# Performance work log

Measured on AMD Instinct MI355X. Metric: run time of the kernel, lower is better.

The kernel has to match this reference:

```python
import jax, jax.numpy as jnp
import numpy as np
from jax import lax

LN_EPS = 1e-5

def _conv1d(h, w, b):
    # h: [N, L, Cin], w: [Cout, Cin, K] (torch Conv1d layout), padding=1
    out = lax.conv_general_dilated(h, w, window_strides=(1,), padding=[(1, 1)],
                                   dimension_numbers=("NWC", "OIW", "NWC"))
    return out + b

def _layer_norm(h, g, b):
    m = jnp.mean(h, axis=-1, keepdims=True)
    v = jnp.mean((h - m) ** 2, axis=-1, keepdims=True)
    return (h - m) * lax.rsqrt(v + LN_EPS) * g + b

def setup_inputs() -> dict:
    key = jax.random.key(0)
    ks = jax.random.split(key, 8)
    N, L, D, F = 32, 512, 384, 256
    return {
        "x": jax.random.normal(ks[0], (N, L, D), jnp.float32),
        "conv1_w": jax.random.normal(ks[1], (F, D, 3), jnp.float32) * 0.05,
        "conv1_b": jnp.zeros((F,), jnp.float32),
        "ln1_g": jnp.ones((F,), jnp.float32),
        "ln1_b": jnp.zeros((F,), jnp.float32),
        "conv2_w": jax.random.normal(ks[2], (F, F, 3), jnp.float32) * 0.05,
        "conv2_b": jnp.zeros((F,), jnp.float32),
        "ln2_g": jnp.ones((F,), jnp.float32),
        "ln2_b": jnp.zeros((F,), jnp.float32),
        "lin_w": jax.random.normal(ks[3], (F,), jnp.float32) * 0.05,
        "lin_b": jnp.zeros((), jnp.float32),
        "target": jax.random.randint(ks[4], (N, L), 0, 8, dtype=jnp.int32),
        "mel_max_length": 2048,
    }

def reference(x, conv1_w, conv1_b, ln1_g, ln1_b, conv2_w, conv2_b, ln2_g, ln2_b,
              lin_w, lin_b, target, mel_max_length):
    # Duration predictor (dropout is identity at inference)
    h = jax.nn.relu(_layer_norm(_conv1d(x, conv1_w, conv1_b), ln1_g, ln1_b))
    h = jax.nn.relu(_layer_norm(_conv1d(h, conv2_w, conv2_b), ln2_g, ln2_b))
    duration_predictor_output = jnp.einsum("nlf,f->nl", h, lin_w) + lin_b  # [N, L]

    # LR: frame t copies phoneme j iff cumsum(dur)[:j] <= t < cumsum(dur)[:j+1]
    # (equivalent to the one-hot alignment matmul, padded to mel_max_length)
    N, L, D = x.shape
    T = mel_max_length
    cums = jnp.cumsum(target, axis=-1)                      # [N, L]
    frames = jnp.arange(T, dtype=cums.dtype)                # [T]
    idx = jax.vmap(lambda c: jnp.searchsorted(c, frames, side="right"))(cums)  # [N, T]
    valid = frames[None, :] < cums[:, -1:]                  # frames beyond total are zero
    gathered = jnp.take_along_axis(x, jnp.clip(idx, 0, L - 1)[:, :, None], axis=1)
    output = gathered * valid[:, :, None].astype(x.dtype)   # [N, T, D]
    return output, duration_predictor_output
```

## Files before the change

kernel.cpp:

```cpp
#include <hip/hip_runtime.h>
#include <hip/hip_bf16.h>

#define NB   32
#define TMEL 2048

typedef unsigned short u16;
typedef short s8v __attribute__((ext_vector_type(8)));
typedef float f4v __attribute__((ext_vector_type(4)));
typedef u16 u16x8 __attribute__((ext_vector_type(8)));

static __device__ __forceinline__ u16 f2bf(float v) {
    __hip_bfloat16 h = __float2bfloat16(v);
    return *(u16*)&h;
}

__global__ __launch_bounds__(256) void gather_prep_kernel(
    const float* __restrict__ x,
    const int*   __restrict__ target,
    const float* __restrict__ w1,
    const float* __restrict__ w2,
    u16* __restrict__ Wt1,
    u16* __restrict__ Wt2,
    u16* __restrict__ zbuf,
    float* __restrict__ out0)
{
    __shared__ int c[512];
    __shared__ int ridx[64];
    const int b = blockIdx.x, tid = threadIdx.x;

    if (b >= 1024) {
        if (b == 1024 && tid < 8) {
            u16x8 z = {0, 0, 0, 0, 0, 0, 0, 0};
            *(u16x8*)(zbuf + tid * 8) = z;
        }
        if (b < 2176) {
            const int K = 1152, DIN = 384;
            int e = (b - 1024) * 256 + tid;
            int f = e / K;
            int rem = e - f * K;
            int kc = rem / DIN;
            int d = rem - kc * DIN;
            Wt1[e] = f2bf(w1[f * K + d * 3 + kc]);
        } else {
            const int K = 768, DIN = 256;
            int e = (b - 2176) * 256 + tid;
            int f = e / K;
            int rem = e - f * K;
            int kc = rem / DIN;
            int d = rem - kc * DIN;
            Wt2[e] = f2bf(w2[f * K + d * 3 + kc]);
        }
        return;
    }

    const int n = b >> 5, sub = b & 31;
    c[tid]       = target[n * 512 + tid];
    c[tid + 256] = target[n * 512 + 256 + tid];
    __syncthreads();
    for (int off = 1; off < 512; off <<= 1) {
        int v0 = (tid       >= off) ? c[tid       - off] : 0;
        int v1 = (tid + 256 >= off) ? c[tid + 256 - off] : 0;
        __syncthreads();
        c[tid]       += v0;
        c[tid + 256] += v1;
        __syncthreads();
    }
    const int total = c[511];
    if (tid < 64) {
        int t = sub * 64 + tid;
        int lo = 0, hi = 512;
        while (lo < hi) {
            int mid = (lo + hi) >> 1;
            if (c[mid] <= t) lo = mid + 1; else hi = mid;
        }
        ridx[tid] = (t < total) ? min(lo, 511) : -1;
    }
    __syncthreads();

    const size_t xbase = (size_t)(n << 9) * 384;
    const size_t obase = ((size_t)(n << 11) + sub * 64) * 384;
    #pragma unroll 4
    for (int it = 0; it < 12; ++it) {
        int u  = tid + it * 256;
        int j  = u % 48;
        int rl = u / 48;
        int ie = ridx[rl];
        f4v v0 = {0.f, 0.f, 0.f, 0.f}, v1 = v0;
        if (ie >= 0) {
            const float* src = &x[xbase + (size_t)ie * 384];
            v0 = *(const f4v*)&src[j * 4];
            v1 = *(const f4v*)&src[(j + 48) * 4];
        }
        float* dst = &out0[obase + (size_t)rl * 384];
        __builtin_nontemporal_store(v0, (f4v*)&dst[j * 4]);
        __builtin_nontemporal_store(v1, (f4v*)&dst[(j + 48) * 4]);
    }
}

template<int DIN, int MODE, int ASRC>
__global__ __launch_bounds__(256, 2) void conv_mfma_kernel(
    const void* __restrict__ Ainp,
    const u16* __restrict__ Wt,
    const float* __restrict__ cb,
    const float* __restrict__ g,
    const float* __restrict__ bb,
    const float* __restrict__ lw,
    const float* __restrict__ lbp,
    const u16* __restrict__ zbuf,
    void* __restrict__ outp)
{
    const int K = 3 * DIN, NT = K / 64;
    __shared__ __align__(128) char AsB[2][32 * 128];
    __shared__ __align__(128) char BsB[2][256 * 128];
    __shared__ float redS[32 * 4];
    __shared__ float redQ[32 * 4];
    __shared__ float redP[32 * 4];

    const int tid  = threadIdx.x;
    const int lane = tid & 63, wc = tid >> 6;
    const int lr = lane & 15, q4 = lane >> 4;
    const int sb = (blockIdx.x & 7) * 64 + (blockIdx.x >> 3);
    const int m0 = sb * 32;
    const int n  = m0 >> 9, l0 = m0 & 511;

    f4v acc[2][4];
    #pragma unroll
    for (int mi = 0; mi < 2; mi++)
        #pragma unroll
        for (int ni = 0; ni < 4; ni++) acc[mi][ni] = {0.f, 0.f, 0.f, 0.f};

    const int a_r    = tid >> 3;
    const int a_slot = (tid & 7) ^ (a_r & 7);
    const int b_r    = tid >> 3;
    const int b_slot = (tid & 7) ^ (b_r & 7);

    const int aoff0 = (lr) * 128;
    const int aoff1 = (16 + lr) * 128;
    int boff[4];
    #pragma unroll
    for (int ni = 0; ni < 4; ni++) boff[ni] = (64 * wc + 16 * ni + lr) * 128;
    const int slot0 = ((q4)     ^ (lr & 7)) << 4;
    const int slot1 = ((q4 | 4) ^ (lr & 7)) << 4;

    auto stage = [&](int buf, int t) {
        const int k0 = t * 64;
        const int kc = k0 / DIN;
        const int d0 = k0 - kc * DIN;
        const int lp = l0 + a_r + kc - 1;
        if (ASRC == 0) {
            f4v v0 = {0.f, 0.f, 0.f, 0.f}, v1 = v0;
            if (lp >= 0 && lp < 512) {
                const float* src = (const float*)Ainp
                    + ((size_t)((n << 9) + lp)) * DIN + d0 + (tid & 7) * 8;
                v0 = *(const f4v*)src;
                v1 = *(const f4v*)(src + 4);
            }
            u16x8 r;
            #pragma unroll
            for (int jj = 0; jj < 4; jj++) { r[jj] = f2bf(v0[jj]); r[4 + jj] = f2bf(v1[jj]); }
            *(u16x8*)(AsB[buf] + a_r * 128 + a_slot * 16) = r;
        } else {
            const u16* asrc = (lp >= 0 && lp < 512)
                ? ((const u16*)Ainp + ((size_t)((n << 9) + lp)) * DIN + d0 + a_slot * 8)
                : zbuf;
            __builtin_amdgcn_global_load_lds(
                (const __attribute__((address_space(1))) void*)asrc,
                (__attribute__((address_space(3))) void*)(AsB[buf] + tid * 16), 16, 0, 0);
        }
        const u16* bsrc = Wt + (size_t)b_r * K + k0 + b_slot * 8;
        #pragma unroll
        for (int q = 0; q < 8; q++) {
            __builtin_amdgcn_global_load_lds(
                (const __attribute__((address_space(1))) void*)(bsrc + (size_t)q * 32 * K),
                (__attribute__((address_space(3))) void*)(BsB[buf] + q * 4096 + tid * 16),
                16, 0, 0);
        }
    };

    auto compute = [&](int buf) {
        #pragma unroll
        for (int kk = 0; kk < 2; kk++) {
            const int sl = kk ? slot1 : slot0;
            s8v a0 = *(const s8v*)(AsB[buf] + aoff0 + sl);
            s8v a1 = *(const s8v*)(AsB[buf] + aoff1 + sl);
            s8v b0 = *(const s8v*)(BsB[buf] + boff[0] + sl);
            s8v b1 = *(const s8v*)(BsB[buf] + boff[1] + sl);
            s8v b2 = *(const s8v*)(BsB[buf] + boff[2] + sl);
            s8v b3 = *(const s8v*)(BsB[buf] + boff[3] + sl);
            acc[0][0] = __builtin_amdgcn_mfma_f32_16x16x32_bf16(a0, b0, acc[0][0], 0, 0, 0);
            acc[0][1] = __builtin_amdgcn_mfma_f32_16x16x32_bf16(a0, b1, acc[0][1], 0, 0, 0);
            acc[0][2] = __builtin_amdgcn_mfma_f32_16x16x32_bf16(a0, b2, acc[0][2], 0, 0, 0);
            acc[0][3] = __builtin_amdgcn_mfma_f32_16x16x32_bf16(a0, b3, acc[0][3], 0, 0, 0);
            acc[1][0] = __builtin_amdgcn_mfma_f32_16x16x32_bf16(a1, b0, acc[1][0], 0, 0, 0);
            acc[1][1] = __builtin_amdgcn_mfma_f32_16x16x32_bf16(a1, b1, acc[1][1], 0, 0, 0);
            acc[1][2] = __builtin_amdgcn_mfma_f32_16x16x32_bf16(a1, b2, acc[1][2], 0, 0, 0);
            acc[1][3] = __builtin_amdgcn_mfma_f32_16x16x32_bf16(a1, b3, acc[1][3], 0, 0, 0);
        }
    };

    stage(0, 0);
    __syncthreads();
    int cur = 0;
    for (int t = 0; t < NT; ++t) {
        if (t + 1 < NT) stage(cur ^ 1, t + 1);
        compute(cur);
        __syncthreads();
        cur ^= 1;
    }

    float cbv[4], gv[4], bbv[4], lwv[4];
    int col[4];
    #pragma unroll
    for (int ni = 0; ni < 4; ni++) {
        col[ni] = 64 * wc + 16 * ni + lr;
        cbv[ni] = cb[col[ni]]; gv[ni] = g[col[ni]]; bbv[ni] = bb[col[ni]];
        if (MODE == 1) lwv[ni] = lw[col[ni]];
    }

    float sv[2][4], sq[2][4];
    #pragma unroll
    for (int mi = 0; mi < 2; mi++)
        #pragma unroll
        for (int reg = 0; reg < 4; reg++) {
            float s = 0.f, q = 0.f;
            #pragma unroll
            for (int ni = 0; ni < 4; ni++) {
                float v = acc[mi][ni][reg] + cbv[ni];
                s += v; q += v * v;
            }
            #pragma unroll
            for (int msk = 1; msk < 16; msk <<= 1) {
                s += __shfl_xor(s, msk);
                q += __shfl_xor(q, msk);
            }
            sv[mi][reg] = s; sq[mi][reg] = q;
        }
    if (lr == 0) {
        #pragma unroll
        for (int mi = 0; mi < 2; mi++)
            #pragma unroll
            for (int reg = 0; reg < 4; reg++) {
                int rl = 16 * mi + 4 * q4 + reg;
                redS[rl * 4 + wc] = sv[mi][reg];
                redQ[rl * 4 + wc] = sq[mi][reg];
            }
    }
    __syncthreads();

    float mean_[2][4], rs_[2][4];
    #pragma unroll
    for (int mi = 0; mi < 2; mi++)
        #pragma unroll
        for (int reg = 0; reg < 4; reg++) {
            int rl = 16 * mi + 4 * q4 + reg;
            float4 ps = *(float4*)&redS[rl * 4];
            float4 pq = *(float4*)&redQ[rl * 4];
            float mean = (ps.x + ps.y + ps.z + ps.w) * (1.f / 256.f);
            float var  = (pq.x + pq.y + pq.z + pq.w) * (1.f / 256.f) - mean * mean;
            mean_[mi][reg] = mean;
            rs_[mi][reg]   = rsqrtf(var + 1e-5f);
        }

    if (MODE == 0) {
        u16* hout = (u16*)outp;
        #pragma unroll
        for (int mi = 0; mi < 2; mi++)
            #pragma unroll
            for (int reg = 0; reg < 4; reg++) {
                int rl = 16 * mi + 4 * q4 + reg;
                #pragma unroll
                for (int ni = 0; ni < 4; ni++) {
                    float v = acc[mi][ni][reg] + cbv[ni];
                    float o = fmaxf(0.f, (v - mean_[mi][reg]) * rs_[mi][reg] * gv[ni] + bbv[ni]);
                    hout[(size_t)(m0 + rl) * 256 + col[ni]] = f2bf(o);
                }
            }
    } else {
        float pp[2][4];
        #pragma unroll
        for (int mi = 0; mi < 2; mi++)
            #pragma unroll
            for (int reg = 0; reg < 4; reg++) {
                float p = 0.f;
                #pragma unroll
                for (int ni = 0; ni < 4; ni++) {
                    float v = acc[mi][ni][reg] + cbv[ni];
                    float o = fmaxf(0.f, (v - mean_[mi][reg]) * rs_[mi][reg] * gv[ni] + bbv[ni]);
                    p += o * lwv[ni];
                }
                #pragma unroll
                for (int msk = 1; msk < 16; msk <<= 1) p += __shfl_xor(p, msk);
                pp[mi][reg] = p;
            }
        if (lr == 0) {
            #pragma unroll
            for (int mi = 0; mi < 2; mi++)
                #pragma unroll
                for (int reg = 0; reg < 4; reg++) {
                    int rl = 16 * mi + 4 * q4 + reg;
                    redP[rl * 4 + wc] = pp[mi][reg];
                }
        }
        __syncthreads();
        if (tid < 32) {
            float* dpo = (float*)outp;
            float4 p4 = *(float4*)&redP[tid * 4];
            dpo[m0 + tid] = p4.x + p4.y + p4.z + p4.w + lbp[0];
        }
    }
}

extern "C" void kernel_launch(void* const* d_in, const int* in_sizes, int n_in,
                              void* d_out, int out_size, void* d_ws, size_t ws_size,
                              hipStream_t stream) {
    const float* x   = (const float*)d_in[0];
    const float* w1  = (const float*)d_in[1];
    const float* b1  = (const float*)d_in[2];
    const float* g1  = (const float*)d_in[3];
    const float* bb1 = (const float*)d_in[4];
    const float* w2  = (const float*)d_in[5];
    const float* b2  = (const float*)d_in[6];
    const float* g2  = (const float*)d_in[7];
    const float* bb2 = (const float*)d_in[8];
    const float* lw  = (const float*)d_in[9];
    const float* lb  = (const float*)d_in[10];
    const int* target = (const int*)d_in[11];

    char* wsb  = (char*)d_ws;
    u16*  zbuf = (u16*)wsb;
    u16*  Wt1  = (u16*)(wsb + 128);
    u16*  Wt2  = (u16*)(wsb + 128 + 589824);
    u16*  h1   = (u16*)(wsb + 128 + 589824 + 393216);

    float* out0 = (float*)d_out;
    float* dpo  = out0 + (size_t)32 * 2048 * 384;

    gather_prep_kernel<<<2944, 256, 0, stream>>>(
        x, target, w1, w2, Wt1, Wt2, zbuf, out0);

    conv_mfma_kernel<384, 0, 0><<<512, 256, 0, stream>>>(
        (const void*)x, Wt1, b1, g1, bb1, nullptr, nullptr, zbuf, (void*)h1);

    conv_mfma_kernel<256, 1, 1><<<512, 256, 0, stream>>>(
        (const void*)h1, Wt2, b2, g2, bb2, lw, lb, zbuf, (void*)dpo);
}
```

Before: 71.56 us.

## Fuse length-regulator gather into the tail of both conv kernels

The length-regulator gather (prefix-sum, binary search, row copy of about 100MB of output) moves out of the prep kernel and into the epilogue of each conv MFMA kernel. Each conv launch handles half of the 65536 output rows and reuses the A-tile shared memory for the scan buffers. The aim is to overlap the bandwidth-bound gather with the compute-bound conv blocks and drop a large separate grid. In exchange it lengthens every conv block and adds extra syncs, which could cut the conv kernels' occupancy or efficiency.

```diff
diff --git a/kernel.cpp b/kernel.cpp
--- a/kernel.cpp
+++ b/kernel.cpp
@@ -14,86 +14,34 @@
     return *(u16*)&h;
 }
 
-__global__ __launch_bounds__(256) void gather_prep_kernel(
-    const float* __restrict__ x,
-    const int*   __restrict__ target,
+__global__ __launch_bounds__(256) void prep_kernel(
     const float* __restrict__ w1,
     const float* __restrict__ w2,
     u16* __restrict__ Wt1,
     u16* __restrict__ Wt2,
-    u16* __restrict__ zbuf,
-    float* __restrict__ out0)
+    u16* __restrict__ zbuf)
 {
-    __shared__ int c[512];
-    __shared__ int ridx[64];
     const int b = blockIdx.x, tid = threadIdx.x;
-
-    if (b >= 1024) {
-        if (b == 1024 && tid < 8) {
-            u16x8 z = {0, 0, 0, 0, 0, 0, 0, 0};
-            *(u16x8*)(zbuf + tid * 8) = z;
-        }
-        if (b < 2176) {
-            const int K = 1152, DIN = 384;
-            int e = (b - 1024) * 256 + tid;
-            int f = e / K;
-            int rem = e - f * K;
-            int kc = rem / DIN;
-            int d = rem - kc * DIN;
-            Wt1[e] = f2bf(w1[f * K + d * 3 + kc]);
-        } else {
-            const int K = 768, DIN = 256;
-            int e = (b - 2176) * 256 + tid;
-            int f = e / K;
-            int rem = e - f * K;
-            int kc = rem / DIN;
-            int d = rem - kc * DIN;
-            Wt2[e] = f2bf(w2[f * K + d * 3 + kc]);
-        }
-        return;
-    }
-
-    const int n = b >> 5, sub = b & 31;
-    c[tid]       = target[n * 512 + tid];
-    c[tid + 256] = target[n * 512 + 256 + tid];
-    __syncthreads();
-    for (int off = 1; off < 512; off <<= 1) {
-        int v0 = (tid       >= off) ? c[tid       - off] : 0;
-        int v1 = (tid + 256 >= off) ? c[tid + 256 - off] : 0;
-        __syncthreads();
-        c[tid]       += v0;
-        c[tid + 256] += v1;
-        __syncthreads();
-    }
-    const int total = c[511];
-    if (tid < 64) {
-        int t = sub * 64 + tid;
-        int lo = 0, hi = 512;
-        while (lo < hi) {
-            int mid = (lo + hi) >> 1;
-            if (c[mid] <= t) lo = mid + 1; else hi = mid;
-        }
-        ridx[tid] = (t < total) ? min(lo, 511) : -1;
-    }
-    __syncthreads();
-
-    const size_t xbase = (size_t)(n << 9) * 384;
-    const size_t obase = ((size_t)(n << 11) + sub * 64) * 384;
-    #pragma unroll 4
-    for (int it = 0; it < 12; ++it) {
-        int u  = tid + it * 256;
-        int j  = u % 48;
-        int rl = u / 48;
-        int ie = ridx[rl];
-        f4v v0 = {0.f, 0.f, 0.f, 0.f}, v1 = v0;
-        if (ie >= 0) {
-            const float* src = &x[xbase + (size_t)ie * 384];
-            v0 = *(const f4v*)&src[j * 4];
-            v1 = *(const f4v*)&src[(j + 48) * 4];
-        }
-        float* dst = &out0[obase + (size_t)rl * 384];
-        __builtin_nontemporal_store(v0, (f4v*)&dst[j * 4]);
-        __builtin_nontemporal_store(v1, (f4v*)&dst[(j + 48) * 4]);
+    if (b == 0 && tid < 8) {
+        u16x8 z = {0, 0, 0, 0, 0, 0, 0, 0};
+        *(u16x8*)(zbuf + tid * 8) = z;
+    }
+    if (b < 1152) {
+        const int K = 1152, DIN = 384;
+        int e = b * 256 + tid;
+        int f = e / K;
+        int rem = e - f * K;
+        int kc = rem / DIN;
+        int d = rem - kc * DIN;
+        Wt1[e] = f2bf(w1[f * K + d * 3 + kc]);
+    } else {
+        const int K = 768, DIN = 256;
+        int e = (b - 1152) * 256 + tid;
+        int f = e / K;
+        int rem = e - f * K;
+        int kc = rem / DIN;
+        int d = rem - kc * DIN;
+        Wt2[e] = f2bf(w2[f * K + d * 3 + kc]);
     }
 }
 
@@ -107,7 +55,11 @@
     const float* __restrict__ lw,
     const float* __restrict__ lbp,
     const u16* __restrict__ zbuf,
-    void* __restrict__ outp)
+    void* __restrict__ outp,
+    const float* __restrict__ xf,
+    const int* __restrict__ target,
+    float* __restrict__ out0,
+    int gbase)
 {
     const int K = 3 * DIN, NT = K / 64;
     __shared__ __align__(128) char AsB[2][32 * 128];
@@ -308,6 +260,53 @@
             dpo[m0 + tid] = p4.x + p4.y + p4.z + p4.w + lbp[0];
         }
     }
+
+    __syncthreads();
+    int* c    = (int*)(AsB[0]);
+    int* ridx = (int*)(AsB[0] + 2048);
+    const int grow0 = gbase + sb * 64;
+    const int ng    = grow0 >> 11;
+    c[tid]       = target[ng * 512 + tid];
+    c[tid + 256] = target[ng * 512 + 256 + tid];
+    __syncthreads();
+    for (int off = 1; off < 512; off <<= 1) {
+        int v0 = (tid       >= off) ? c[tid       - off] : 0;
+        int v1 = (tid + 256 >= off) ? c[tid + 256 - off] : 0;
+        __syncthreads();
+        c[tid]       += v0;
+        c[tid + 256] += v1;
+        __syncthreads();
+    }
+    const int total = c[511];
+    if (tid < 64) {
+        int t = (grow0 & 2047) + tid;
+        int lo = 0, hi = 512;
+        while (lo < hi) {
+            int mid = (lo + hi) >> 1;
+            if (c[mid] <= t) lo = mid + 1; else hi = mid;
+        }
+        ridx[tid] = (t < total) ? min(lo, 511) : -1;
+    }
+    __syncthreads();
+
+    const size_t xbase = (size_t)(ng << 9) * 384;
+    const size_t obase = (size_t)grow0 * 384;
+    #pragma unroll 4
+    for (int it = 0; it < 12; ++it) {
+        int u  = tid + it * 256;
+        int j  = u % 48;
+        int rl = u / 48;
+        int ie = ridx[rl];
+        f4v v0 = {0.f, 0.f, 0.f, 0.f}, v1 = v0;
+        if (ie >= 0) {
+            const float* src = &xf[xbase + (size_t)ie * 384];
+            v0 = *(const f4v*)&src[j * 4];
+            v1 = *(const f4v*)&src[(j + 48) * 4];
+        }
+        float* dst = &out0[obase + (size_t)rl * 384];
+        __builtin_nontemporal_store(v0, (f4v*)&dst[j * 4]);
+        __builtin_nontemporal_store(v1, (f4v*)&dst[(j + 48) * 4]);
+    }
 }
 
 extern "C" void kernel_launch(void* const* d_in, const int* in_sizes, int n_in,
@@ -335,12 +334,13 @@
     float* out0 = (float*)d_out;
     float* dpo  = out0 + (size_t)32 * 2048 * 384;
 
-    gather_prep_kernel<<<2944, 256, 0, stream>>>(
-        x, target, w1, w2, Wt1, Wt2, zbuf, out0);
+    prep_kernel<<<1920, 256, 0, stream>>>(w1, w2, Wt1, Wt2, zbuf);
 
     conv_mfma_kernel<384, 0, 0><<<512, 256, 0, stream>>>(
-        (const void*)x, Wt1, b1, g1, bb1, nullptr, nullptr, zbuf, (void*)h1);
+        (const void*)x, Wt1, b1, g1, bb1, nullptr, nullptr, zbuf, (void*)h1,
+        x, target, out0, 0);
 
     conv_mfma_kernel<256, 1, 1><<<512, 256, 0, stream>>>(
-        (const void*)h1, Wt2, b2, g2, bb2, lw, lb, zbuf, (void*)dpo);
+        (const void*)h1, Wt2, b2, g2, bb2, lw, lb, zbuf, (void*)dpo,
+        x, target, out0, 32768);
 }
```

Result: slower. 74.18 us (+3.7%).

## Fuse both conv+LayerNorm stages into one kernel with halo recompute

Applied to the files above, without the earlier changes.

Merges the two conv MFMA kernels into a single kernel. Each block computes conv1 over 48 rows, which covers its 32 output rows plus a halo, and keeps the normalized bf16 h1 tile in LDS for conv2. This removes the h1 global round-trip, one kernel launch and the zero-buffer setup. In exchange it does 1.5x the conv1 MFMA work, conv2 weight staging is no longer double-buffered, and LDS use rises to about 78KB, which may limit occupancy.

```diff
diff --git a/kernel.cpp b/kernel.cpp
--- a/kernel.cpp
+++ b/kernel.cpp
@@ -1,8 +1,5 @@
 #include <hip/hip_runtime.h>
 #include <hip/hip_bf16.h>
-
-#define NB   32
-#define TMEL 2048
 
 typedef unsigned short u16;
 typedef short s8v __attribute__((ext_vector_type(8)));
@@ -21,7 +18,6 @@
     const float* __restrict__ w2,
     u16* __restrict__ Wt1,
     u16* __restrict__ Wt2,
-    u16* __restrict__ zbuf,
     float* __restrict__ out0)
 {
     __shared__ int c[512];
@@ -29,10 +25,6 @@
     const int b = blockIdx.x, tid = threadIdx.x;
 
     if (b >= 1024) {
-        if (b == 1024 && tid < 8) {
-            u16x8 z = {0, 0, 0, 0, 0, 0, 0, 0};
-            *(u16x8*)(zbuf + tid * 8) = z;
-        }
         if (b < 2176) {
             const int K = 1152, DIN = 384;
             int e = (b - 1024) * 256 + tid;
@@ -97,24 +89,21 @@
     }
 }
 
-template<int DIN, int MODE, int ASRC>
-__global__ __launch_bounds__(256, 2) void conv_mfma_kernel(
-    const void* __restrict__ Ainp,
-    const u16* __restrict__ Wt,
-    const float* __restrict__ cb,
-    const float* __restrict__ g,
-    const float* __restrict__ bb,
-    const float* __restrict__ lw,
-    const float* __restrict__ lbp,
-    const u16* __restrict__ zbuf,
-    void* __restrict__ outp)
+__global__ __launch_bounds__(256, 2) void fused_conv_kernel(
+    const float* __restrict__ x,
+    const u16* __restrict__ Wt1,
+    const u16* __restrict__ Wt2,
+    const float* __restrict__ cb1, const float* __restrict__ g1,
+    const float* __restrict__ bb1,
+    const float* __restrict__ cb2, const float* __restrict__ g2,
+    const float* __restrict__ bb2,
+    const float* __restrict__ lw, const float* __restrict__ lbp,
+    float* __restrict__ dpo)
 {
-    const int K = 3 * DIN, NT = K / 64;
-    __shared__ __align__(128) char AsB[2][32 * 128];
-    __shared__ __align__(128) char BsB[2][256 * 128];
-    __shared__ float redS[32 * 4];
-    __shared__ float redQ[32 * 4];
-    __shared__ float redP[32 * 4];
+    __shared__ __align__(128) char LDS[79872];
+    float* redS = (float*)(LDS + 77824);
+    float* redQ = (float*)(LDS + 78592);
+    float* redP = (float*)(LDS + 79360);
 
     const int tid  = threadIdx.x;
     const int lane = tid & 63, wc = tid >> 6;
@@ -123,70 +112,63 @@
     const int m0 = sb * 32;
     const int n  = m0 >> 9, l0 = m0 & 511;
 
-    f4v acc[2][4];
-    #pragma unroll
-    for (int mi = 0; mi < 2; mi++)
-        #pragma unroll
-        for (int ni = 0; ni < 4; ni++) acc[mi][ni] = {0.f, 0.f, 0.f, 0.f};
-
-    const int a_r    = tid >> 3;
-    const int a_slot = (tid & 7) ^ (a_r & 7);
     const int b_r    = tid >> 3;
     const int b_slot = (tid & 7) ^ (b_r & 7);
-
-    const int aoff0 = (lr) * 128;
-    const int aoff1 = (16 + lr) * 128;
     int boff[4];
     #pragma unroll
     for (int ni = 0; ni < 4; ni++) boff[ni] = (64 * wc + 16 * ni + lr) * 128;
     const int slot0 = ((q4)     ^ (lr & 7)) << 4;
     const int slot1 = ((q4 | 4) ^ (lr & 7)) << 4;
 
-    auto stage = [&](int buf, int t) {
+    f4v acc[3][4];
+    #pragma unroll
+    for (int mi = 0; mi < 3; mi++)
+        #pragma unroll
+        for (int ni = 0; ni < 4; ni++) acc[mi][ni] = {0.f, 0.f, 0.f, 0.f};
+
+    auto stage1 = [&](int buf, int t) {
         const int k0 = t * 64;
-        const int kc = k0 / DIN;
-        const int d0 = k0 - kc * DIN;
-        const int lp = l0 + a_r + kc - 1;
-        if (ASRC == 0) {
+        const int kc = k0 / 384;
+        const int d0 = k0 - kc * 384;
+        char* As = LDS + 65536 + buf * 6144;
+        for (int u = tid; u < 384; u += 256) {
+            int ar = u >> 3;
+            int aslot = (u & 7) ^ (ar & 7);
+            int lp = l0 - 8 + ar + kc - 1;
             f4v v0 = {0.f, 0.f, 0.f, 0.f}, v1 = v0;
             if (lp >= 0 && lp < 512) {
-                const float* src = (const float*)Ainp
-                    + ((size_t)((n << 9) + lp)) * DIN + d0 + (tid & 7) * 8;
+                const float* src = x + ((size_t)((n << 9) + lp)) * 384 + d0 + (u & 7) * 8;
                 v0 = *(const f4v*)src;
                 v1 = *(const f4v*)(src + 4);
             }
             u16x8 r;
             #pragma unroll
             for (int jj = 0; jj < 4; jj++) { r[jj] = f2bf(v0[jj]); r[4 + jj] = f2bf(v1[jj]); }
-            *(u16x8*)(AsB[buf] + a_r * 128 + a_slot * 16) = r;
-        } else {
-            const u16* asrc = (lp >= 0 && lp < 512)
-                ? ((const u16*)Ainp + ((size_t)((n << 9) + lp)) * DIN + d0 + a_slot * 8)
-                : zbuf;
-            __builtin_amdgcn_global_load_lds(
-                (const __attribute__((address_space(1))) void*)asrc,
-                (__attribute__((address_space(3))) void*)(AsB[buf] + tid * 16), 16, 0, 0);
-        }
-        const u16* bsrc = Wt + (size_t)b_r * K + k0 + b_slot * 8;
+            *(u16x8*)(As + ar * 128 + aslot * 16) = r;
+        }
+        const u16* bsrc = Wt1 + (size_t)b_r * 1152 + k0 + b_slot * 8;
         #pragma unroll
         for (int q = 0; q < 8; q++) {
             __builtin_amdgcn_global_load_lds(
-                (const __attribute__((address_space(1))) void*)(bsrc + (size_t)q * 32 * K),
-                (__attribute__((address_space(3))) void*)(BsB[buf] + q * 4096 + tid * 16),
+                (const __attribute__((address_space(1))) void*)(bsrc + (size_t)q * 32 * 1152),
+                (__attribute__((address_space(3))) void*)(LDS + buf * 32768 + q * 4096 + tid * 16),
                 16, 0, 0);
         }
     };
 
-    auto compute = [&](int buf) {
+    auto compute1 = [&](int buf) {
+        char* As = LDS + 65536 + buf * 6144;
+        char* Bs = LDS + buf * 32768;
         #pragma unroll
         for (int kk = 0; kk < 2; kk++) {
             const int sl = kk ? slot1 : slot0;
-            s8v a0 = *(const s8v*)(AsB[buf] + aoff0 + sl);
-            s8v a1 = *(const s8v*)(AsB[buf] + aoff1 + sl);
-            s8v b0 = *(const s8v*)(BsB[buf] + boff[0] + sl);
-            s8v b1 = *(const s8v*)(BsB[buf] + boff[1] + sl);
-            s8v b2 = *(const s8v*)(BsB[buf] + boff[2] + sl);
-            s8v b3 = *(const s8v*)(BsB[buf] + boff[3] + sl);
+            s8v a0 = *(const s8v*)(As + (lr) * 128 + sl);
+            s8v a1 = *(const s8v*)(As + (16 + lr) * 128 + sl);
+            s8v a2 = *(const s8v*)(As + (32 + lr) * 128 + sl);
+            s8v b0 = *(const s8v*)(Bs + boff[0] + sl);
+            s8v b1 = *(const s8v*)(Bs + boff[1] + sl);
+            s8v b2 = *(const s8v*)(Bs + boff[2] + sl);
+            s8v b3 = *(const s8v*)(Bs + boff[3] + sl);
             acc[0][0] = __builtin_amdgcn_mfma_f32_16x16x32_bf16(a0, b0, acc[0][0], 0, 0, 0);
             acc[0][1] = __builtin_amdgcn_mfma_f32_16x16x32_bf16(a0, b1, acc[0][1], 0, 0, 0);
             acc[0][2] = __builtin_amdgcn_mfma_f32_16x16x32_bf16(a0, b2, acc[0][2], 0, 0, 0);
@@ -195,31 +177,33 @@
             acc[1][1] = __builtin_amdgcn_mfma_f32_16x16x32_bf16(a1, b1, acc[1][1], 0, 0, 0);
             acc[1][2] = __builtin_amdgcn_mfma_f32_16x16x32_bf16(a1, b2, acc[1][2], 0, 0, 0);
             acc[1][3] = __builtin_amdgcn_mfma_f32_16x16x32_bf16(a1, b3, acc[1][3], 0, 0, 0);
+            acc[2][0] = __builtin_amdgcn_mfma_f32_16x16x32_bf16(a2, b0, acc[2][0], 0, 0, 0);
+            acc[2][1] = __builtin_amdgcn_mfma_f32_16x16x32_bf16(a2, b1, acc[2][1], 0, 0, 0);
+            acc[2][2] = __builtin_amdgcn_mfma_f32_16x16x32_bf16(a2, b2, acc[2][2], 0, 0, 0);
+            acc[2][3] = __builtin_amdgcn_mfma_f32_16x16x32_bf16(a2, b3, acc[2][3], 0, 0, 0);
         }
     };
 
-    stage(0, 0);
+    stage1(0, 0);
     __syncthreads();
     int cur = 0;
-    for (int t = 0; t < NT; ++t) {
-        if (t + 1 < NT) stage(cur ^ 1, t + 1);
-        compute(cur);
+    for (int t = 0; t < 18; ++t) {
+        if (t + 1 < 18) stage1(cur ^ 1, t + 1);
+        compute1(cur);
         __syncthreads();
         cur ^= 1;
     }
 
-    float cbv[4], gv[4], bbv[4], lwv[4];
     int col[4];
+    float cbv[4], gv[4], bbv[4];
     #pragma unroll
     for (int ni = 0; ni < 4; ni++) {
         col[ni] = 64 * wc + 16 * ni + lr;
-        cbv[ni] = cb[col[ni]]; gv[ni] = g[col[ni]]; bbv[ni] = bb[col[ni]];
-        if (MODE == 1) lwv[ni] = lw[col[ni]];
-    }
-
-    float sv[2][4], sq[2][4];
-    #pragma unroll
-    for (int mi = 0; mi < 2; mi++)
+        cbv[ni] = cb1[col[ni]]; gv[ni] = g1[col[ni]]; bbv[ni] = bb1[col[ni]];
+    }
+
+    #pragma unroll
+    for (int mi = 0; mi < 3; mi++)
         #pragma unroll
         for (int reg = 0; reg < 4; reg++) {
             float s = 0.f, q = 0.f;
@@ -233,8 +217,112 @@
                 s += __shfl_xor(s, msk);
                 q += __shfl_xor(q, msk);
             }
+            if (lr == 0) {
+                int rl = 16 * mi + 4 * q4 + reg;
+                redS[rl * 4 + wc] = s;
+                redQ[rl * 4 + wc] = q;
+            }
+        }
+    __syncthreads();
+
+    #pragma unroll
+    for (int mi = 0; mi < 3; mi++)
+        #pragma unroll
+        for (int reg = 0; reg < 4; reg++) {
+            int rl = 16 * mi + 4 * q4 + reg;
+            int h  = rl - 7;
+            if (h >= 0 && h < 34) {
+                float4 ps = *(float4*)&redS[rl * 4];
+                float4 pq = *(float4*)&redQ[rl * 4];
+                float mean = (ps.x + ps.y + ps.z + ps.w) * (1.f / 256.f);
+                float var  = (pq.x + pq.y + pq.z + pq.w) * (1.f / 256.f) - mean * mean;
+                float rs   = rsqrtf(var + 1e-5f);
+                int l = l0 - 8 + rl;
+                bool lv = (l >= 0 && l < 512);
+                #pragma unroll
+                for (int ni = 0; ni < 4; ni++) {
+                    float v = acc[mi][ni][reg] + cbv[ni];
+                    float o = lv ? fmaxf(0.f, (v - mean) * rs * gv[ni] + bbv[ni]) : 0.f;
+                    int slot = (col[ni] >> 3) ^ (h & 7);
+                    *(u16*)(LDS + h * 512 + slot * 16 + (col[ni] & 7) * 2) = f2bf(o);
+                }
+            }
+        }
+
+    f4v acc2[2][4];
+    #pragma unroll
+    for (int mi = 0; mi < 2; mi++)
+        #pragma unroll
+        for (int ni = 0; ni < 4; ni++) acc2[mi][ni] = {0.f, 0.f, 0.f, 0.f};
+
+    for (int t2 = 0; t2 < 12; ++t2) {
+        __syncthreads();
+        const int k0 = t2 * 64;
+        const u16* bsrc = Wt2 + (size_t)b_r * 768 + k0 + b_slot * 8;
+        #pragma unroll
+        for (int q = 0; q < 8; q++) {
+            __builtin_amdgcn_global_load_lds(
+                (const __attribute__((address_space(1))) void*)(bsrc + (size_t)q * 32 * 768),
+                (__attribute__((address_space(3))) void*)(LDS + 32768 + q * 4096 + tid * 16),
+                16, 0, 0);
+        }
+        __syncthreads();
+
+        const int kc2   = t2 >> 2;
+        const int sbase = 8 * (t2 & 3);
+        #pragma unroll
+        for (int kk = 0; kk < 2; kk++) {
+            const int sl = kk ? slot1 : slot0;
+            char* Bs = LDS + 32768;
+            s8v b0 = *(const s8v*)(Bs + boff[0] + sl);
+            s8v b1 = *(const s8v*)(Bs + boff[1] + sl);
+            s8v b2 = *(const s8v*)(Bs + boff[2] + sl);
+            s8v b3 = *(const s8v*)(Bs + boff[3] + sl);
+            s8v a0, a1;
+            {
+                int h = lr + kc2;
+                int s = sbase + 4 * kk + q4;
+                a0 = *(const s8v*)(LDS + h * 512 + ((s ^ (h & 7)) << 4));
+                h = 16 + lr + kc2;
+                a1 = *(const s8v*)(LDS + h * 512 + ((s ^ (h & 7)) << 4));
+            }
+            acc2[0][0] = __builtin_amdgcn_mfma_f32_16x16x32_bf16(a0, b0, acc2[0][0], 0, 0, 0);
+            acc2[0][1] = __builtin_amdgcn_mfma_f32_16x16x32_bf16(a0, b1, acc2[0][1], 0, 0, 0);
+            acc2[0][2] = __builtin_amdgcn_mfma_f32_16x16x32_bf16(a0, b2, acc2[0][2], 0, 0, 0);
+            acc2[0][3] = __builtin_amdgcn_mfma_f32_16x16x32_bf16(a0, b3, acc2[0][3], 0, 0, 0);
+            acc2[1][0] = __builtin_amdgcn_mfma_f32_16x16x32_bf16(a1, b0, acc2[1][0], 0, 0, 0);
+            acc2[1][1] = __builtin_amdgcn_mfma_f32_16x16x32_bf16(a1, b1, acc2[1][1], 0, 0, 0);
+            acc2[1][2] = __builtin_amdgcn_mfma_f32_16x16x32_bf16(a1, b2, acc2[1][2], 0, 0, 0);
+            acc2[1][3] = __builtin_amdgcn_mfma_f32_16x16x32_bf16(a1, b3, acc2[1][3], 0, 0, 0);
+        }
+    }
+
+    float cbv2[4], gv2[4], bbv2[4], lwv[4];
+    #pragma unroll
+    for (int ni = 0; ni < 4; ni++) {
+        cbv2[ni] = cb2[col[ni]]; gv2[ni] = g2[col[ni]]; bbv2[ni] = bb2[col[ni]];
+        lwv[ni]  = lw[col[ni]];
+    }
+
+    float sv[2][4], sq[2][4];
+    #pragma unroll
+    for (int mi = 0; mi < 2; mi++)
+        #pragma unroll
+        for (int reg = 0; reg < 4; reg++) {
+            float s = 0.f, q = 0.f;
+            #pragma unroll
+            for (int ni = 0; ni < 4; ni++) {
+                float v = acc2[mi][ni][reg] + cbv2[ni];
+                s += v; q += v * v;
+            }
+            #pragma unroll
+            for (int msk = 1; msk < 16; msk <<= 1) {
+                s += __shfl_xor(s, msk);
+                q += __shfl_xor(q, msk);
+            }
             sv[mi][reg] = s; sq[mi][reg] = q;
         }
+    __syncthreads();
     if (lr == 0) {
         #pragma unroll
         for (int mi = 0; mi < 2; mi++)
@@ -247,7 +335,7 @@
     }
     __syncthreads();
 
-    float mean_[2][4], rs_[2][4];
+    float pp[2][4];
     #pragma unroll
     for (int mi = 0; mi < 2; mi++)
         #pragma unroll
@@ -257,56 +345,31 @@
             float4 pq = *(float4*)&redQ[rl * 4];
             float mean = (ps.x + ps.y + ps.z + ps.w) * (1.f / 256.f);
             float var  = (pq.x + pq.y + pq.z + pq.w) * (1.f / 256.f) - mean * mean;
-            mean_[mi][reg] = mean;
-            rs_[mi][reg]   = rsqrtf(var + 1e-5f);
-        }
-
-    if (MODE == 0) {
-        u16* hout = (u16*)outp;
+            float rs   = rsqrtf(var + 1e-5f);
+            float p = 0.f;
+            #pragma unroll
+            for (int ni = 0; ni < 4; ni++) {
+                float v = acc2[mi][ni][reg] + cbv2[ni];
+                float o = fmaxf(0.f, (v - mean) * rs * gv2[ni] + bbv2[ni]);
+                p += o * lwv[ni];
+            }
+            #pragma unroll
+            for (int msk = 1; msk < 16; msk <<= 1) p += __shfl_xor(p, msk);
+            pp[mi][reg] = p;
+        }
+    if (lr == 0) {
         #pragma unroll
         for (int mi = 0; mi < 2; mi++)
             #pragma unroll
             for (int reg = 0; reg < 4; reg++) {
                 int rl = 16 * mi + 4 * q4 + reg;
-                #pragma unroll
-                for (int ni = 0; ni < 4; ni++) {
-                    float v = acc[mi][ni][reg] + cbv[ni];
-                    float o = fmaxf(0.f, (v - mean_[mi][reg]) * rs_[mi][reg] * gv[ni] + bbv[ni]);
-                    hout[(size_t)(m0 + rl) * 256 + col[ni]] = f2bf(o);
-                }
-            }
-    } else {
-        float pp[2][4];
-        #pragma unroll
-        for (int mi = 0; mi < 2; mi++)
-            #pragma unroll
-            for (int reg = 0; reg < 4; reg++) {
-                float p = 0.f;
-                #pragma unroll
-                for (int ni = 0; ni < 4; ni++) {
-                    float v = acc[mi][ni][reg] + cbv[ni];
-                    float o = fmaxf(0.f, (v - mean_[mi][reg]) * rs_[mi][reg] * gv[ni] + bbv[ni]);
-                    p += o * lwv[ni];
-                }
-                #pragma unroll
-                for (int msk = 1; msk < 16; msk <<= 1) p += __shfl_xor(p, msk);
-                pp[mi][reg] = p;
-            }
-        if (lr == 0) {
-            #pragma unroll
-            for (int mi = 0; mi < 2; mi++)
-                #pragma unroll
-                for (int reg = 0; reg < 4; reg++) {
-                    int rl = 16 * mi + 4 * q4 + reg;
-                    redP[rl * 4 + wc] = pp[mi][reg];
-                }
-        }
-        __syncthreads();
-        if (tid < 32) {
-            float* dpo = (float*)outp;
-            float4 p4 = *(float4*)&redP[tid * 4];
-            dpo[m0 + tid] = p4.x + p4.y + p4.z + p4.w + lbp[0];
-        }
+                redP[rl * 4 + wc] = pp[mi][reg];
+            }
+    }
+    __syncthreads();
+    if (tid < 32) {
+        float4 p4 = *(float4*)&redP[tid * 4];
+        dpo[m0 + tid] = p4.x + p4.y + p4.z + p4.w + lbp[0];
     }
 }
 
@@ -326,21 +389,16 @@
     const float* lb  = (const float*)d_in[10];
     const int* target = (const int*)d_in[11];
 
-    char* wsb  = (char*)d_ws;
-    u16*  zbuf = (u16*)wsb;
-    u16*  Wt1  = (u16*)(wsb + 128);
-    u16*  Wt2  = (u16*)(wsb + 128 + 589824);
-    u16*  h1   = (u16*)(wsb + 128 + 589824 + 393216);
+    char* wsb = (char*)d_ws;
+    u16*  Wt1 = (u16*)wsb;
+    u16*  Wt2 = (u16*)(wsb + 589824);
 
     float* out0 = (float*)d_out;
     float* dpo  = out0 + (size_t)32 * 2048 * 384;
 
     gather_prep_kernel<<<2944, 256, 0, stream>>>(
-        x, target, w1, w2, Wt1, Wt2, zbuf, out0);
-
-    conv_mfma_kernel<384, 0, 0><<<512, 256, 0, stream>>>(
-        (const void*)x, Wt1, b1, g1, bb1, nullptr, nullptr, zbuf, (void*)h1);
-
-    conv_mfma_kernel<256, 1, 1><<<512, 256, 0, stream>>>(
-        (const void*)h1, Wt2, b2, g2, bb2, lw, lb, zbuf, (void*)dpo);
+        x, target, w1, w2, Wt1, Wt2, out0);
+
+    fused_conv_kernel<<<512, 256, 0, stream>>>(
+        x, Wt1, Wt2, b1, g1, bb1, b2, g2, bb2, lw, lb, dpo);
 }
```

After: 70.10 us. -2.0%, faster.
